# Optimization experiments

Hardware: AMD Instinct MI355X
Metric: run time of the kernel (lower is better)

## Reference

```python
import jax, jax.numpy as jnp
import numpy as np

B, L, DIM, HEADS, DIM_HEAD = 16, 1024, 512, 8, 64


def _make_perms(rng):
    # perm = identity on first DIM indices, random permutation of [DIM, L*DIM) after
    perms = []
    for _ in range(HEADS - 1):
        tail = rng.permutation(np.arange(DIM, L * DIM))
        perms.append(np.concatenate([np.arange(DIM), tail]))
    return jnp.asarray(np.stack(perms), dtype=jnp.int64)


def setup_inputs() -> dict:
    key = jax.random.key(0)
    ks = jax.random.split(key, 6)
    s = 0.02
    return {
        "x": jax.random.normal(ks[0], (B, L, DIM), dtype=jnp.float32),
        "perms": _make_perms(np.random.default_rng(0)),
        "Wq": jax.random.normal(ks[1], (HEADS, DIM, DIM_HEAD), dtype=jnp.float32) * s,
        "Wk": jax.random.normal(ks[2], (HEADS, DIM, DIM_HEAD), dtype=jnp.float32) * s,
        "Wv": jax.random.normal(ks[3], (HEADS, DIM, DIM_HEAD), dtype=jnp.float32) * s,
        "Wo": jax.random.normal(ks[4], (DIM, HEADS * DIM_HEAD), dtype=jnp.float32) * s,
        "bo": jnp.zeros((DIM,), dtype=jnp.float32),
    }


def reference(x, perms, Wq, Wk, Wv, Wo, bo):
    b, l, d = x.shape
    h, _, e = Wq.shape
    scale = e ** -0.5
    # shuffled query inputs for heads 1..h-1
    flat = x.reshape(b, l * d)                      # [B, L*D]
    shuf = flat[:, perms].reshape(b, h - 1, l, d)   # [B, H-1, L, D]
    xq = jnp.concatenate([x[:, None], shuf], axis=1)  # [B, H, L, D]
    q = jnp.einsum('bhld,hde->bhle', xq, Wq)
    k = jnp.einsum('bld,hde->bhle', x, Wk)
    v = jnp.einsum('bld,hde->bhle', x, Wv)
    attn = jax.nn.softmax(jnp.einsum('bhqe,bhke->bhqk', q, k) * scale, axis=-1)
    out = jnp.einsum('bhqk,bhke->bhqe', attn, v)    # [B, H, L, E]
    out = out.transpose(0, 2, 1, 3).reshape(b, l, h * e)  # concat heads on last dim
    return jnp.einsum('bli,di->bld', out, Wo) + bo
```

## Files before the change

kernel.cpp:

```cpp
#include <hip/hip_runtime.h>

#define LL 1024
#define DD 512
#define HH 8
#define EE 64
#define LDX (LL*DD)
#define BB 16

typedef _Float16 h8 __attribute__((ext_vector_type(8)));
typedef _Float16 h4 __attribute__((ext_vector_type(4)));
typedef float f4 __attribute__((ext_vector_type(4)));
typedef int i4 __attribute__((ext_vector_type(4)));

__device__ __forceinline__ f4 mfma16(h8 a, h8 b, f4 c) {
    return __builtin_amdgcn_mfma_f32_16x16x32_f16(a, b, c, 0, 0, 0);
}

__global__ __launch_bounds__(256) void k_prep_all(
    const float* __restrict__ x,  const float* __restrict__ Wq,
    const float* __restrict__ Wk, const float* __restrict__ Wv,
    const float* __restrict__ Wo,
    _Float16* __restrict__ xT, _Float16* __restrict__ x16,
    _Float16* __restrict__ WT, _Float16* __restrict__ Wo16)
{
    const int bx = blockIdx.x;
    const int t = threadIdx.x;
    if (bx < 2048) {
        const int s = bx * 256 + t;
        h8 lo, hi;
        #pragma unroll
        for (int b = 0; b < 8; ++b)  lo[b] = (_Float16)x[(size_t)b*LDX + s];
        #pragma unroll
        for (int b = 0; b < 8; ++b)  hi[b] = (_Float16)x[(size_t)(b+8)*LDX + s];
        _Float16* d = xT + (size_t)s * BB;
        *(h8*)d = lo; *(h8*)(d + 8) = hi;
        #pragma unroll
        for (int b = 0; b < 8; ++b)  x16[(size_t)b*LDX + s]     = lo[b];
        #pragma unroll
        for (int b = 0; b < 8; ++b)  x16[(size_t)(b+8)*LDX + s] = hi[b];
    } else if (bx < 2048 + 192) {
        const int id = bx - 2048;
        const int d0 = (id & 7) * 64;
        const int zz = id >> 3;
        const float* src; float sc = 1.f;
        if (zz < 8)       src = Wk + (size_t)zz*DD*EE;
        else if (zz < 16) src = Wv + (size_t)(zz-8)*DD*EE;
        else            { src = Wq + (size_t)(zz-16)*DD*EE; sc = 0.18033688011112042f; }
        const int e = t & 63, dq = t >> 6;
        #pragma unroll
        for (int i = 0; i < 16; ++i) {
            int d = d0 + dq*16 + i;
            WT[(size_t)(zz*64 + e)*DD + d] = (_Float16)(src[(size_t)d*EE + e] * sc);
        }
    } else {
        const int i = (bx - (2048 + 192)) * 256 + t;
        f4 v = ((const f4*)Wo)[i];
        #pragma unroll
        for (int j = 0; j < 4; ++j) Wo16[4*i + j] = (_Float16)v[j];
    }
}

__device__ __forceinline__ void qkv_body(
    int y, int r0,
    const _Float16* __restrict__ x16, const _Float16* __restrict__ WT,
    _Float16* __restrict__ qw, _Float16* __restrict__ kw, _Float16* __restrict__ vw,
    _Float16* smem)
{
    auto As = (_Float16(*)[128][72])smem;
    auto Bs = (_Float16(*)[128][72])(smem + 2*128*72);

    const int t = threadIdx.x;
    const int wv = t >> 6, lane = t & 63;
    const int m = lane & 15, qd = lane >> 4;
    const int sr = t >> 1, sc0 = (t & 1) * 32;

    const _Float16* ax = x16 + (size_t)(r0 + sr)*DD + sc0;
    const _Float16* bx = WT  + (size_t)(y*128 + sr)*DD + sc0;

    #pragma unroll
    for (int c = 0; c < 4; ++c) {
        *(h8*)&As[0][sr][sc0 + 8*c] = *(const h8*)(ax + 8*c);
        *(h8*)&Bs[0][sr][sc0 + 8*c] = *(const h8*)(bx + 8*c);
    }
    __syncthreads();

    f4 acc[2][8] = {};
    int cur = 0;
    for (int kt = 0; kt < 8; ++kt) {
        const int alt = cur ^ 1;
        h8 an[4], bn[4];
        if (kt < 7) {
            const _Float16* a2 = ax + (kt+1)*64;
            const _Float16* b2 = bx + (kt+1)*64;
            #pragma unroll
            for (int c = 0; c < 4; ++c) {
                an[c] = *(const h8*)(a2 + 8*c);
                bn[c] = *(const h8*)(b2 + 8*c);
            }
        }
        #pragma unroll
        for (int ks = 0; ks < 2; ++ks) {
            h8 a0 = *(const h8*)&As[cur][32*wv +  0 + m][32*ks + 8*qd];
            h8 a1 = *(const h8*)&As[cur][32*wv + 16 + m][32*ks + 8*qd];
            #pragma unroll
            for (int nt = 0; nt < 8; ++nt) {
                h8 bb = *(const h8*)&Bs[cur][16*nt + m][32*ks + 8*qd];
                acc[0][nt] = mfma16(a0, bb, acc[0][nt]);
                acc[1][nt] = mfma16(a1, bb, acc[1][nt]);
            }
        }
        if (kt < 7) {
            #pragma unroll
            for (int c = 0; c < 4; ++c) {
                *(h8*)&As[alt][sr][sc0 + 8*c] = an[c];
                *(h8*)&Bs[alt][sr][sc0 + 8*c] = bn[c];
            }
            __syncthreads();
            cur = alt;
        }
    }

    #pragma unroll
    for (int nt = 0; nt < 8; ++nt) {
        const int n = y*128 + 16*nt + m;
        const int z = n >> 6, e = n & 63;
        if (z >= 17) continue;
        _Float16* dst; int h;
        if (z < 8)       { dst = kw; h = z; }
        else if (z < 16) { dst = vw; h = z - 8; }
        else             { dst = qw; h = 0; }
        dst += (size_t)h*LL*EE + e;
        #pragma unroll
        for (int mt = 0; mt < 2; ++mt)
            #pragma unroll
            for (int r = 0; r < 4; ++r) {
                int R = r0 + 32*wv + 16*mt + 4*qd + r;
                int b = R >> 10, l = R & 1023;
                dst[((size_t)b*HH*LL + l)*EE] = (_Float16)acc[mt][nt][r];
            }
    }
}

__device__ __forceinline__ void qshuf_body(
    int l0, int h,
    const _Float16* __restrict__ xT, const int* __restrict__ perms,
    const _Float16* __restrict__ WT, _Float16* __restrict__ qw,
    _Float16* smem)
{
    auto As = (_Float16(*)[64][72])smem;
    auto Bs = (_Float16(*)[64][72])(smem + 2*64*72);

    const _Float16* Wb = WT + (size_t)((16 + h)*64)*DD;
    const int* pbase = perms + (size_t)(h-1)*LDX;

    const int t = threadIdx.x;
    const int wv = t >> 6, lane = t & 63;
    const int m = lane & 15, qd = lane >> 4;
    const int lg = t >> 6, kcol = t & 63;
    const int br = t >> 2, bc0 = (t & 3) * 16;

    int pv[8];
    #pragma unroll
    for (int kt = 0; kt < 8; ++kt)
        pv[kt] = pbase[(size_t)(l0 + lg)*DD + kt*64 + kcol];

    h8 g0p[3], g1p[3], b0p[3], b1p[3];
    #pragma unroll
    for (int j = 0; j < 3; ++j) {
        const _Float16* g = xT + (size_t)pv[j] * BB;
        g0p[j] = *(const h8*)g; g1p[j] = *(const h8*)(g + 8);
        const _Float16* s = Wb + (size_t)br*DD + j*64 + bc0;
        b0p[j] = *(const h8*)s; b1p[j] = *(const h8*)(s + 8);
    }

    *(h8*)&Bs[0][br][bc0]     = b0p[0];
    *(h8*)&Bs[0][br][bc0 + 8] = b1p[0];
    #pragma unroll
    for (int i = 0; i < 8; ++i) As[0][lg*16 + i][kcol]     = g0p[0][i];
    #pragma unroll
    for (int i = 0; i < 8; ++i) As[0][lg*16 + 8 + i][kcol] = g1p[0][i];
    __syncthreads();

    f4 acc[4] = {};
    #pragma unroll
    for (int kt = 0; kt < 8; ++kt) {
        const int cur = kt & 1;
        if (kt + 3 < 8) {
            const int st = (kt + 3) % 3;
            const _Float16* g = xT + (size_t)pv[kt+3] * BB;
            g0p[st] = *(const h8*)g; g1p[st] = *(const h8*)(g + 8);
            const _Float16* s = Wb + (size_t)br*DD + (kt+3)*64 + bc0;
            b0p[st] = *(const h8*)s; b1p[st] = *(const h8*)(s + 8);
        }
        #pragma unroll
        for (int ks = 0; ks < 2; ++ks) {
            h8 a = *(const h8*)&As[cur][16*wv + m][32*ks + 8*qd];
            #pragma unroll
            for (int nt = 0; nt < 4; ++nt) {
                h8 bb = *(const h8*)&Bs[cur][16*nt + m][32*ks + 8*qd];
                acc[nt] = mfma16(a, bb, acc[nt]);
            }
        }
        if (kt < 7) {
            const int alt = cur ^ 1;
            const int st = (kt + 1) % 3;
            *(h8*)&Bs[alt][br][bc0]     = b0p[st];
            *(h8*)&Bs[alt][br][bc0 + 8] = b1p[st];
            #pragma unroll
            for (int i = 0; i < 8; ++i) As[alt][lg*16 + i][kcol]     = g0p[st][i];
            #pragma unroll
            for (int i = 0; i < 8; ++i) As[alt][lg*16 + 8 + i][kcol] = g1p[st][i];
            __syncthreads();
        }
    }

    #pragma unroll
    for (int nt = 0; nt < 4; ++nt)
        #pragma unroll
        for (int r = 0; r < 4; ++r) {
            int b = 4*qd + r;
            qw[((size_t)(b*HH + h)*LL + l0 + wv)*EE + 16*nt + m] = (_Float16)acc[nt][r];
        }
}

__global__ __launch_bounds__(256) void k_qkv_qshuf(
    const _Float16* __restrict__ x16, const _Float16* __restrict__ xT,
    const int* __restrict__ perms, const _Float16* __restrict__ WT,
    _Float16* __restrict__ qw, _Float16* __restrict__ kw, _Float16* __restrict__ vw)
{
    __shared__ __align__(16) _Float16 smem[4*128*72];
    const int bx = blockIdx.x;
    const int lx = (bx & 7) * 368 + (bx >> 3);
    const int g = lx / 23, pos = lx % 23;
    if (pos < 9) {
        const int qid = g*9 + pos;
        qkv_body(qid % 9, (qid / 9) * 128, x16, WT, qw, kw, vw, smem);
    } else {
        const int sid = g*14 + (pos - 9);
        qshuf_body((sid & 255) * 4, (sid >> 8) + 1, xT, perms, WT, qw, smem);
    }
}

__global__ __launch_bounds__(512, 2) void k_attn(
    const _Float16* __restrict__ qw, const _Float16* __restrict__ kw,
    const _Float16* __restrict__ vw, _Float16* __restrict__ oa)
{
    const int bh = blockIdx.x;
    const int l0 = blockIdx.y * 256;
    const int b = bh >> 3, h = bh & 7;
    const _Float16* qb = qw + ((size_t)bh*LL + l0)*EE;
    const _Float16* kb = kw + (size_t)bh*LL*EE;
    const _Float16* vb = vw + (size_t)bh*LL*EE;

    __shared__ __align__(16) _Float16 KsF[4][64*64];
    __shared__ __align__(16) _Float16 VtsF[4][64*64];

    const int t = threadIdx.x;
    const int wv = t >> 6, lane = t & 63;
    const int m = lane & 15, qd = lane >> 4;
    const int m7 = m & 7;
    const int qdp = ((qd & 1) << 1) | (qd >> 1);
    const int krow = t >> 3, c0 = t & 7;
    const int vkey = t & 63, vec = t >> 6;
    const int vhi = vkey >> 3, vlo = vkey & 7;

    h8 qa[2][2];
    #pragma unroll
    for (int mt = 0; mt < 2; ++mt)
        #pragma unroll
        for (int ks = 0; ks < 2; ++ks)
            qa[mt][ks] = *(const h8*)(qb + (size_t)(32*wv + 16*mt + m)*EE + 32*ks + 8*qd);

    f4 oacc[2][4] = {};
    f4 lpacc[2] = {};
    h8 ones;
    #pragma unroll
    for (int i = 0; i < 8; ++i) ones[i] = (_Float16)1.f;

    auto loadK = [&](int kt) -> h8 {
        return *(const h8*)(kb + (size_t)(kt*64 + krow)*EE + 8*c0);
    };
    auto loadV = [&](int kt) -> h8 {
        return *(const h8*)(vb + (size_t)(kt*64 + vkey)*EE + 8*vec);
    };
    auto stageK = [&](int buf, h8 kr) {
        *(h8*)&KsF[buf][(krow<<6) + 8*(c0 ^ (krow & 7))] = kr;
    };
    auto stageV = [&](int buf, h8 vr) {
        #pragma unroll
        for (int i = 0; i < 8; ++i)
            VtsF[buf][((8*vec + i)<<6) + 8*(vhi ^ i) + vlo] = vr[i];
    };
    auto compute = [&](int buf) {
        f4 sacc[2][4] = {};
        __builtin_amdgcn_s_setprio(1);
        #pragma unroll
        for (int ks = 0; ks < 2; ++ks)
            #pragma unroll
            for (int nt = 0; nt < 4; ++nt) {
                h8 kf = *(const h8*)&KsF[buf][((16*nt + m)<<6) + 8*((4*ks + qd) ^ m7)];
                sacc[0][nt] = mfma16(kf, qa[0][ks], sacc[0][nt]);
                sacc[1][nt] = mfma16(kf, qa[1][ks], sacc[1][nt]);
            }
        __builtin_amdgcn_s_setprio(0);

        unsigned E[2][4][2];
        #pragma unroll
        for (int mt = 0; mt < 2; ++mt)
            #pragma unroll
            for (int nt = 0; nt < 4; ++nt) {
                float e0 = __builtin_amdgcn_exp2f(sacc[mt][nt][0]);
                float e1 = __builtin_amdgcn_exp2f(sacc[mt][nt][1]);
                float e2 = __builtin_amdgcn_exp2f(sacc[mt][nt][2]);
                float e3 = __builtin_amdgcn_exp2f(sacc[mt][nt][3]);
                E[mt][nt][0] = __builtin_bit_cast(unsigned, __builtin_amdgcn_cvt_pkrtz(e0, e1));
                E[mt][nt][1] = __builtin_bit_cast(unsigned, __builtin_amdgcn_cvt_pkrtz(e2, e3));
            }

        h8 pa[2][2];
        #pragma unroll
        for (int mt = 0; mt < 2; ++mt)
            #pragma unroll
            for (int ks = 0; ks < 2; ++ks) {
                auto xx = __builtin_amdgcn_permlane16_swap(E[mt][2*ks][0], E[mt][2*ks+1][0], false, false);
                auto yy = __builtin_amdgcn_permlane16_swap(E[mt][2*ks][1], E[mt][2*ks+1][1], false, false);
                i4 pw;
                pw[0] = (int)xx[0]; pw[1] = (int)yy[0]; pw[2] = (int)xx[1]; pw[3] = (int)yy[1];
                pa[mt][ks] = __builtin_bit_cast(h8, pw);
            }

        __builtin_amdgcn_s_setprio(1);
        #pragma unroll
        for (int ks = 0; ks < 2; ++ks) {
            #pragma unroll
            for (int nt = 0; nt < 4; ++nt) {
                h8 vf = *(const h8*)&VtsF[buf][((16*nt + m)<<6) + 8*((4*ks + qdp) ^ m7)];
                oacc[0][nt] = mfma16(pa[0][ks], vf, oacc[0][nt]);
                oacc[1][nt] = mfma16(pa[1][ks], vf, oacc[1][nt]);
            }
            lpacc[0] = mfma16(pa[0][ks], ones, lpacc[0]);
            lpacc[1] = mfma16(pa[1][ks], ones, lpacc[1]);
        }
        __builtin_amdgcn_s_setprio(0);
    };

    {
        h8 k0 = loadK(0), v0 = loadV(0), k1 = loadK(1), v1 = loadV(1);
        stageK(0, k0); stageV(0, v0);
        stageK(1, k1); stageV(1, v1);
    }
    __syncthreads();

    #pragma unroll
    for (int j = 0; j < 8; ++j) {
        h8 ka, va, kc, vc;
        if (j < 7) {
            ka = loadK(2*j + 2); va = loadV(2*j + 2);
            kc = loadK(2*j + 3); vc = loadV(2*j + 3);
        }
        compute((2*j) & 3);
        if (j < 7) { stageK((2*j + 2) & 3, ka); stageV((2*j + 2) & 3, va); }
        compute((2*j + 1) & 3);
        if (j < 7) {
            stageK((2*j + 3) & 3, kc); stageV((2*j + 3) & 3, vc);
            __syncthreads();
        }
    }

    _Float16* ob = oa + ((size_t)(b*LL + l0))*(HH*EE) + h*EE;
    #pragma unroll
    for (int mt = 0; mt < 2; ++mt)
        #pragma unroll
        for (int r = 0; r < 4; ++r) {
            const float inv = __builtin_amdgcn_rcpf(lpacc[mt][r]);
            #pragma unroll
            for (int nt = 0; nt < 4; ++nt) {
                int row = 32*wv + 16*mt + 4*qd + r;
                ob[(size_t)row*(HH*EE) + 16*nt + m] = (_Float16)(oacc[mt][nt][r] * inv);
            }
        }
}

__global__ __launch_bounds__(256) void k_oproj(
    const _Float16* __restrict__ oa, const _Float16* __restrict__ Wo16,
    const float* __restrict__ bo, float* __restrict__ out)
{
    const int lid = ((int)blockIdx.x & 7) * 64 + ((int)blockIdx.x >> 3);
    const int y  = lid & 3;
    const int r0 = (lid >> 2) * 128;

    __shared__ __align__(16) _Float16 As[2][128][72];
    __shared__ __align__(16) _Float16 Bs[2][128][72];

    const int t = threadIdx.x;
    const int wv = t >> 6, lane = t & 63;
    const int m = lane & 15, qd = lane >> 4;
    const int sr = t >> 1, sc0 = (t & 1) * 32;

    const _Float16* ax = oa   + (size_t)(r0 + sr)*DD + sc0;
    const _Float16* bx = Wo16 + (size_t)(y*128 + sr)*DD + sc0;

    #pragma unroll
    for (int c = 0; c < 4; ++c) {
        *(h8*)&As[0][sr][sc0 + 8*c] = *(const h8*)(ax + 8*c);
        *(h8*)&Bs[0][sr][sc0 + 8*c] = *(const h8*)(bx + 8*c);
    }
    __syncthreads();

    f4 acc[2][8] = {};
    int cur = 0;
    for (int kt = 0; kt < 8; ++kt) {
        const int alt = cur ^ 1;
        h8 an[4], bn[4];
        if (kt < 7) {
            const _Float16* a2 = ax + (kt+1)*64;
            const _Float16* b2 = bx + (kt+1)*64;
            #pragma unroll
            for (int c = 0; c < 4; ++c) {
                an[c] = *(const h8*)(a2 + 8*c);
                bn[c] = *(const h8*)(b2 + 8*c);
            }
        }
        #pragma unroll
        for (int ks = 0; ks < 2; ++ks) {
            h8 a0 = *(const h8*)&As[cur][32*wv +  0 + m][32*ks + 8*qd];
            h8 a1 = *(const h8*)&As[cur][32*wv + 16 + m][32*ks + 8*qd];
            #pragma unroll
            for (int nt = 0; nt < 8; ++nt) {
                h8 bb = *(const h8*)&Bs[cur][16*nt + m][32*ks + 8*qd];
                acc[0][nt] = mfma16(a0, bb, acc[0][nt]);
                acc[1][nt] = mfma16(a1, bb, acc[1][nt]);
            }
        }
        if (kt < 7) {
            #pragma unroll
            for (int c = 0; c < 4; ++c) {
                *(h8*)&As[alt][sr][sc0 + 8*c] = an[c];
                *(h8*)&Bs[alt][sr][sc0 + 8*c] = bn[c];
            }
            __syncthreads();
            cur = alt;
        }
    }

    #pragma unroll
    for (int nt = 0; nt < 8; ++nt) {
        const int col = y*128 + 16*nt + m;
        const float bias = bo[col];
        #pragma unroll
        for (int mt = 0; mt < 2; ++mt)
            #pragma unroll
            for (int r = 0; r < 4; ++r) {
                int row = 32*wv + 16*mt + 4*qd + r;
                out[(size_t)(r0 + row)*DD + col] = acc[mt][nt][r] + bias;
            }
    }
}

extern "C" void kernel_launch(void* const* d_in, const int* in_sizes, int n_in,
                              void* d_out, int out_size, void* d_ws, size_t ws_size,
                              hipStream_t stream)
{
    const float* x  = (const float*)d_in[0];
    const int*   pm = (const int*)d_in[1];
    const float* Wq = (const float*)d_in[2];
    const float* Wk = (const float*)d_in[3];
    const float* Wv = (const float*)d_in[4];
    const float* Wo = (const float*)d_in[5];
    const float* bo = (const float*)d_in[6];
    float* out = (float*)d_out;

    const size_t QS = (size_t)BB * HH * LL * EE;
    _Float16* x16  = (_Float16*)d_out;
    _Float16* q    = (_Float16*)d_out + QS;
    _Float16* k    = (_Float16*)d_ws;
    _Float16* v    = k + QS;
    _Float16* oaw  = v + QS;
    _Float16* xT   = oaw;
    _Float16* WT   = oaw + QS;
    _Float16* Wo16 = WT + (size_t)24*64*DD;

    k_prep_all <<<dim3(2048 + 192 + 256), 256, 0, stream>>>(
        x, Wq, Wk, Wv, Wo, xT, x16, WT, Wo16);
    k_qkv_qshuf<<<dim3(2944),          256, 0, stream>>>(x16, xT, pm, WT, q, k, v);
    k_attn     <<<dim3(BB*HH, LL/256), 512, 0, stream>>>(q, k, v, oaw);
    k_oproj    <<<dim3(512),           256, 0, stream>>>(oaw, Wo16, bo, out);
}
```

Measured before the change: 245.5 us.

## Double attention block to 1024 threads and split K/V staging across halves

The attention kernel now runs 1024-thread blocks that each cover 512 query rows, halving the grid. Each K/V tile is loaded into shared memory once per block and reused by twice as many query waves. The first 512 threads stage K and the other 512 stage V, so each thread does one load and one store per tile instead of two. The trade-offs are fewer blocks (256) relative to the CU count, a wider barrier, and a launch bound of 4 that may force register spills or not be met.

```diff
diff --git a/kernel.cpp b/kernel.cpp
--- a/kernel.cpp
+++ b/kernel.cpp
@@ -241,12 +241,12 @@
     }
 }
 
-__global__ __launch_bounds__(512, 2) void k_attn(
+__global__ __launch_bounds__(1024, 4) void k_attn(
     const _Float16* __restrict__ qw, const _Float16* __restrict__ kw,
     const _Float16* __restrict__ vw, _Float16* __restrict__ oa)
 {
     const int bh = blockIdx.x;
-    const int l0 = blockIdx.y * 256;
+    const int l0 = blockIdx.y * 512;
     const int b = bh >> 3, h = bh & 7;
     const _Float16* qb = qw + ((size_t)bh*LL + l0)*EE;
     const _Float16* kb = kw + (size_t)bh*LL*EE;
@@ -260,8 +260,10 @@
     const int m = lane & 15, qd = lane >> 4;
     const int m7 = m & 7;
     const int qdp = ((qd & 1) << 1) | (qd >> 1);
-    const int krow = t >> 3, c0 = t & 7;
-    const int vkey = t & 63, vec = t >> 6;
+    const bool isK = (t < 512);
+    const int u = t & 511;
+    const int krow = u >> 3, c0 = u & 7;
+    const int vkey = u & 63, vec = u >> 6;
     const int vhi = vkey >> 3, vlo = vkey & 7;
 
     h8 qa[2][2];
@@ -277,19 +279,18 @@
     #pragma unroll
     for (int i = 0; i < 8; ++i) ones[i] = (_Float16)1.f;
 
-    auto loadK = [&](int kt) -> h8 {
-        return *(const h8*)(kb + (size_t)(kt*64 + krow)*EE + 8*c0);
+    auto loadKV = [&](int kt) -> h8 {
+        if (isK) return *(const h8*)(kb + (size_t)(kt*64 + krow)*EE + 8*c0);
+        else     return *(const h8*)(vb + (size_t)(kt*64 + vkey)*EE + 8*vec);
     };
-    auto loadV = [&](int kt) -> h8 {
-        return *(const h8*)(vb + (size_t)(kt*64 + vkey)*EE + 8*vec);
-    };
-    auto stageK = [&](int buf, h8 kr) {
-        *(h8*)&KsF[buf][(krow<<6) + 8*(c0 ^ (krow & 7))] = kr;
-    };
-    auto stageV = [&](int buf, h8 vr) {
-        #pragma unroll
-        for (int i = 0; i < 8; ++i)
-            VtsF[buf][((8*vec + i)<<6) + 8*(vhi ^ i) + vlo] = vr[i];
+    auto stageKV = [&](int buf, h8 r) {
+        if (isK) {
+            *(h8*)&KsF[buf][(krow<<6) + 8*(c0 ^ (krow & 7))] = r;
+        } else {
+            #pragma unroll
+            for (int i = 0; i < 8; ++i)
+                VtsF[buf][((8*vec + i)<<6) + 8*(vhi ^ i) + vlo] = r[i];
+        }
     };
     auto compute = [&](int buf) {
         f4 sacc[2][4] = {};
@@ -345,24 +346,24 @@
     };
 
     {
-        h8 k0 = loadK(0), v0 = loadV(0), k1 = loadK(1), v1 = loadV(1);
-        stageK(0, k0); stageV(0, v0);
-        stageK(1, k1); stageV(1, v1);
+        h8 r0 = loadKV(0), r1 = loadKV(1);
+        stageKV(0, r0);
+        stageKV(1, r1);
     }
     __syncthreads();
 
     #pragma unroll
     for (int j = 0; j < 8; ++j) {
-        h8 ka, va, kc, vc;
+        h8 ra, rc;
         if (j < 7) {
-            ka = loadK(2*j + 2); va = loadV(2*j + 2);
-            kc = loadK(2*j + 3); vc = loadV(2*j + 3);
+            ra = loadKV(2*j + 2);
+            rc = loadKV(2*j + 3);
         }
         compute((2*j) & 3);
-        if (j < 7) { stageK((2*j + 2) & 3, ka); stageV((2*j + 2) & 3, va); }
+        if (j < 7) stageKV((2*j + 2) & 3, ra);
         compute((2*j + 1) & 3);
         if (j < 7) {
-            stageK((2*j + 3) & 3, kc); stageV((2*j + 3) & 3, vc);
+            stageKV((2*j + 3) & 3, rc);
             __syncthreads();
         }
     }
@@ -482,7 +483,7 @@
 
     k_prep_all <<<dim3(2048 + 192 + 256), 256, 0, stream>>>(
         x, Wq, Wk, Wv, Wo, xT, x16, WT, Wo16);
-    k_qkv_qshuf<<<dim3(2944),          256, 0, stream>>>(x16, xT, pm, WT, q, k, v);
-    k_attn     <<<dim3(BB*HH, LL/256), 512, 0, stream>>>(q, k, v, oaw);
-    k_oproj    <<<dim3(512),           256, 0, stream>>>(oaw, Wo16, bo, out);
-}
+    k_qkv_qshuf<<<dim3(2944),          256,  0, stream>>>(x16, xT, pm, WT, q, k, v);
+    k_attn     <<<dim3(BB*HH, LL/512), 1024, 0, stream>>>(q, k, v, oaw);
+    k_oproj    <<<dim3(512),           256,  0, stream>>>(oaw, Wo16, bo, out);
+}
```

Measured after the change: 240.2 us. 2.2% less time.
